# Performance work log

Hardware: AMD Instinct MI355X
Metric: run time of the kernel (lower is better)

## Reference

```python
import jax, jax.numpy as jnp
import numpy as np

N = 50000
E = 800000
DIM_H = 128
EPS = 1e-5


def _glorot(key, shape):
    fan_in, fan_out = shape[0], shape[1]
    lim = np.sqrt(6.0 / (fan_in + fan_out))
    return jax.random.uniform(key, shape, jnp.float32, -lim, lim)


def setup_inputs() -> dict:
    key = jax.random.key(0)
    ks = jax.random.split(key, 12)
    h = jax.random.normal(ks[0], (N, DIM_H), jnp.float32)
    x = jax.random.normal(ks[1], (N, 3), jnp.float32)
    e = jax.random.randint(ks[2], (2, E), 0, N, jnp.int32)
    dx = jax.random.normal(ks[3], (E, 3), jnp.float32)
    d2 = jax.random.uniform(ks[4], (E, 1), jnp.float32)
    # message_layer.phi params: Linear(2*dim_h+1, dim_h), LayerNorm(dim_h), Linear(dim_h, dim_h)
    W1 = _glorot(ks[5], (2 * DIM_H + 1, DIM_H))
    b1 = jnp.zeros((DIM_H,), jnp.float32)
    g1 = jnp.ones((DIM_H,), jnp.float32)
    beta1 = jnp.zeros((DIM_H,), jnp.float32)
    W2 = _glorot(ks[6], (DIM_H, DIM_H))
    b2 = jnp.zeros((DIM_H,), jnp.float32)
    # outer phi params: Linear(dim_h, dim_h), Linear(dim_h, 1)
    W3 = _glorot(ks[7], (DIM_H, DIM_H))
    b3 = jnp.zeros((DIM_H,), jnp.float32)
    W4 = _glorot(ks[8], (DIM_H, 1))
    b4 = jnp.zeros((1,), jnp.float32)
    return {"h": h, "x": x, "e": e, "dx": dx, "d2": d2,
            "W1": W1, "b1": b1, "g1": g1, "beta1": beta1,
            "W2": W2, "b2": b2, "W3": W3, "b3": b3, "W4": W4, "b4": b4}


def _layernorm(z, g, b):
    mu = jnp.mean(z, axis=-1, keepdims=True)
    var = jnp.mean(jnp.square(z - mu), axis=-1, keepdims=True)
    return (z - mu) * jax.lax.rsqrt(var + EPS) * g + b


def reference(h, x, e, dx, d2, W1, b1, g1, beta1, W2, b2, W3, b3, W4, b4):
    ei, ej = e[0], e[1]
    hi = h[ei]                      # [E, dim_h]
    hj = h[ej]                      # [E, dim_h]
    msg = jnp.concatenate((hi, hj, d2), axis=-1)   # [E, 2*dim_h+1]
    msg = jax.nn.silu(msg @ W1 + b1)
    msg = _layernorm(msg, g1, beta1)
    msg = jax.nn.silu(msg @ W2 + b2)               # [E, dim_h]
    scale = jax.nn.silu(msg @ W3 + b3) @ W4 + b4   # [E, 1]
    vec = dx * scale                               # [E, 3]
    agg = jax.ops.segment_sum(vec, ei, num_segments=N)  # [N, 3]
    return x + agg
```

## Files before the change

### kernel.cpp

```cpp
#include <hip/hip_runtime.h>
#include <hip/hip_bf16.h>
#include <cstdint>

#define NN 50000
#define NE 800000
#define DH 128
#define TILES 50000

typedef __bf16 bf16;
typedef __bf16 bf16x8 __attribute__((ext_vector_type(8)));
typedef float  f32x4  __attribute__((ext_vector_type(4)));

__device__ __forceinline__ float fast_silu(float x) {
    float e = __expf(-x);
    return x * __builtin_amdgcn_rcpf(1.0f + e);
}

__global__ void prep_kernel(const float* __restrict__ W1, const float* __restrict__ W2,
                            const float* __restrict__ W3, const float* __restrict__ b1,
                            const float* __restrict__ g1, const float* __restrict__ bt1,
                            const float* __restrict__ b2, const float* __restrict__ b3,
                            const float* __restrict__ W4,
                            bf16* __restrict__ w1aT, bf16* __restrict__ w1bT,
                            bf16* __restrict__ w2T,  bf16* __restrict__ w3T,
                            float* __restrict__ smalls) {
    int i = blockIdx.x * 256 + threadIdx.x;
    int n = i >> 7, k = i & 127;
    w1aT[i] = (bf16)W1[k * DH + n];
    w1bT[i] = (bf16)W1[(k + DH) * DH + n];
    w2T[i]  = (bf16)W2[k * DH + n];
    w3T[i]  = (bf16)W3[k * DH + n];
    if (i < DH) {
        smalls[i]          = W1[256 * DH + i];
        smalls[DH + i]     = b1[i];
        smalls[2 * DH + i] = g1[i];
        smalls[3 * DH + i] = bt1[i];
        smalls[4 * DH + i] = b2[i];
        smalls[5 * DH + i] = b3[i];
        smalls[6 * DH + i] = W4[i];
    }
}

__global__ __launch_bounds__(256) void node_kernel(const float* __restrict__ h,
                                                   const bf16* __restrict__ w1aT,
                                                   const bf16* __restrict__ w1bT,
                                                   bf16* __restrict__ An,
                                                   bf16* __restrict__ Bn) {
    int lane = threadIdx.x & 63, wid = threadIdx.x >> 6;
    int r = lane & 15, g = lane >> 4;
    int wt = blockIdx.x * 4 + wid;
    if (wt >= (NN / 16)) return;
    int base = wt * 16;
    int node = base + r;

    bf16x8 ha[4];
#pragma unroll
    for (int s = 0; s < 4; s++) {
        const float* hp = h + (size_t)node * DH + s * 32 + g * 8;
        float4 p0 = *(const float4*)hp;
        float4 p1 = *(const float4*)(hp + 4);
        ha[s][0] = (bf16)p0.x; ha[s][1] = (bf16)p0.y;
        ha[s][2] = (bf16)p0.z; ha[s][3] = (bf16)p0.w;
        ha[s][4] = (bf16)p1.x; ha[s][5] = (bf16)p1.y;
        ha[s][6] = (bf16)p1.z; ha[s][7] = (bf16)p1.w;
    }
#pragma unroll
    for (int t = 0; t < 16; t++) {
        const bf16* wmat = (t < 8) ? w1aT : w1bT;
        int n = (t & 7) * 16 + r;
        f32x4 acc = {0.f, 0.f, 0.f, 0.f};
#pragma unroll
        for (int s = 0; s < 4; s++) {
            bf16x8 wb = *(const bf16x8*)(wmat + n * DH + s * 32 + g * 8);
            acc = __builtin_amdgcn_mfma_f32_16x16x32_bf16(ha[s], wb, acc, 0, 0, 0);
        }
        bf16* dst = (t < 8) ? An : Bn;
#pragma unroll
        for (int jj = 0; jj < 4; jj++)
            dst[(size_t)(base + g * 4 + jj) * DH + (t & 7) * 16 + r] = (bf16)acc[jj];
    }
}

__global__ void init_kernel(const float* __restrict__ x, float* __restrict__ out, int n) {
    int i = blockIdx.x * 256 + threadIdx.x;
    if (i < n) out[i] = x[i];
}

__global__ __launch_bounds__(512, 2) void edge_kernel(
    const bf16* __restrict__ An, const bf16* __restrict__ Bn,
    const bf16* __restrict__ w2T, const bf16* __restrict__ w3T,
    const float* __restrict__ smalls, const float* __restrict__ b4p,
    const int* __restrict__ e, const float* __restrict__ dxv,
    const float* __restrict__ d2, float* __restrict__ out) {
    __shared__ __align__(16) bf16 sW2[128 * 136];
    __shared__ __align__(16) bf16 sW3[128 * 136];
    __shared__ __align__(16) bf16 sY[8 * 16 * 136];
    __shared__ float sSm[7 * 128];

    int tid = threadIdx.x;
    for (int c = tid; c < 2048; c += 512) {
        int row = c >> 4, col = (c & 15) * 8;
        *(bf16x8*)&sW2[row * 136 + col] = *(const bf16x8*)&w2T[row * 128 + col];
        *(bf16x8*)&sW3[row * 136 + col] = *(const bf16x8*)&w3T[row * 128 + col];
    }
    if (tid < 128) {
#pragma unroll
        for (int a = 0; a < 7; a++) sSm[a * 128 + tid] = smalls[a * 128 + tid];
    }
    __syncthreads();

    const float* s_w1c = sSm;
    const float* s_b1  = sSm + 128;
    const float* s_g1  = sSm + 256;
    const float* s_bt1 = sSm + 384;
    const float* s_b2  = sSm + 512;
    const float* s_b3  = sSm + 640;
    const float* s_W4  = sSm + 768;
    float b4v = b4p[0];

    int lane = tid & 63, wid = tid >> 6;
    int r = lane & 15, g = lane >> 4;
    bf16* yw = &sY[wid * 16 * 136];
    int wgid = blockIdx.x * 8 + wid;
    int nw = gridDim.x * 8;

    for (int tile = wgid; tile < TILES; tile += nw) {
        int base = tile * 16;
        int ei = e[base + r];
        int ej = e[NE + base + r];
        float d2v = d2[base + r];
        const bf16* Ar = An + (size_t)ei * DH;
        const bf16* Br = Bn + (size_t)ej * DH;

        float z[4][8];
#pragma unroll
        for (int s = 0; s < 4; s++) {
            bf16x8 av = *(const bf16x8*)(Ar + s * 32 + g * 8);
            bf16x8 bv = *(const bf16x8*)(Br + s * 32 + g * 8);
#pragma unroll
            for (int j = 0; j < 8; j++) {
                int f = s * 32 + g * 8 + j;
                float zz = (float)av[j] + (float)bv[j] + d2v * s_w1c[f] + s_b1[f];
                z[s][j] = fast_silu(zz);
            }
        }
        float sum = 0.f, sq = 0.f;
#pragma unroll
        for (int s = 0; s < 4; s++)
#pragma unroll
            for (int j = 0; j < 8; j++) { sum += z[s][j]; sq += z[s][j] * z[s][j]; }
        sum += __shfl_xor(sum, 16); sq += __shfl_xor(sq, 16);
        sum += __shfl_xor(sum, 32); sq += __shfl_xor(sq, 32);
        float mu = sum * 0.0078125f;
        float var = sq * 0.0078125f - mu * mu;
        float rs = __builtin_amdgcn_rsqf(var + 1e-5f);

        bf16x8 af[4];
#pragma unroll
        for (int s = 0; s < 4; s++)
#pragma unroll
            for (int j = 0; j < 8; j++) {
                int f = s * 32 + g * 8 + j;
                af[s][j] = (bf16)((z[s][j] - mu) * rs * s_g1[f] + s_bt1[f]);
            }

#pragma unroll
        for (int t = 0; t < 8; t++) {
            f32x4 acc = {0.f, 0.f, 0.f, 0.f};
#pragma unroll
            for (int s = 0; s < 4; s++) {
                bf16x8 wb = *(const bf16x8*)&sW2[(t * 16 + r) * 136 + s * 32 + g * 8];
                acc = __builtin_amdgcn_mfma_f32_16x16x32_bf16(af[s], wb, acc, 0, 0, 0);
            }
            int n = t * 16 + r;
            float b2n = s_b2[n];
#pragma unroll
            for (int jj = 0; jj < 4; jj++)
                yw[(g * 4 + jj) * 136 + n] = (bf16)fast_silu(acc[jj] + b2n);
        }
        bf16x8 a2[4];
#pragma unroll
        for (int s = 0; s < 4; s++)
            a2[s] = *(const bf16x8*)&yw[r * 136 + s * 32 + g * 8];

        float part[4] = {0.f, 0.f, 0.f, 0.f};
#pragma unroll
        for (int t = 0; t < 8; t++) {
            f32x4 acc = {0.f, 0.f, 0.f, 0.f};
#pragma unroll
            for (int s = 0; s < 4; s++) {
                bf16x8 wb = *(const bf16x8*)&sW3[(t * 16 + r) * 136 + s * 32 + g * 8];
                acc = __builtin_amdgcn_mfma_f32_16x16x32_bf16(a2[s], wb, acc, 0, 0, 0);
            }
            int n = t * 16 + r;
            float b3n = s_b3[n], w4n = s_W4[n];
#pragma unroll
            for (int jj = 0; jj < 4; jj++)
                part[jj] += fast_silu(acc[jj] + b3n) * w4n;
        }
#pragma unroll
        for (int jj = 0; jj < 4; jj++) {
            part[jj] += __shfl_xor(part[jj], 1);
            part[jj] += __shfl_xor(part[jj], 2);
            part[jj] += __shfl_xor(part[jj], 4);
            part[jj] += __shfl_xor(part[jj], 8);
        }
#pragma unroll
        for (int jj = 0; jj < 4; jj++) {
            float scale = part[jj] + b4v;
            int m = g * 4 + jj;
            int eim = __shfl(ei, m);
            if (r < 3)
                atomicAdd(&out[(size_t)eim * 3 + r],
                          dxv[(size_t)(base + m) * 3 + r] * scale);
        }
    }
}

extern "C" void kernel_launch(void* const* d_in, const int* in_sizes, int n_in,
                              void* d_out, int out_size, void* d_ws, size_t ws_size,
                              hipStream_t stream) {
    const float* h   = (const float*)d_in[0];
    const float* x   = (const float*)d_in[1];
    const int*   e   = (const int*)d_in[2];
    const float* dxv = (const float*)d_in[3];
    const float* d2  = (const float*)d_in[4];
    const float* W1  = (const float*)d_in[5];
    const float* b1  = (const float*)d_in[6];
    const float* g1  = (const float*)d_in[7];
    const float* bt1 = (const float*)d_in[8];
    const float* W2  = (const float*)d_in[9];
    const float* b2  = (const float*)d_in[10];
    const float* W3  = (const float*)d_in[11];
    const float* b3  = (const float*)d_in[12];
    const float* W4  = (const float*)d_in[13];
    const float* b4  = (const float*)d_in[14];

    char* ws = (char*)d_ws;
    bf16* An    = (bf16*)(ws);
    bf16* Bn    = (bf16*)(ws + 12800000);
    bf16* w1aT  = (bf16*)(ws + 25600000);
    bf16* w1bT  = (bf16*)(ws + 25600000 + 32768);
    bf16* w2T   = (bf16*)(ws + 25600000 + 65536);
    bf16* w3T   = (bf16*)(ws + 25600000 + 98304);
    float* smalls = (float*)(ws + 25600000 + 131072);
    float* out  = (float*)d_out;

    prep_kernel<<<64, 256, 0, stream>>>(W1, W2, W3, b1, g1, bt1, b2, b3, W4,
                                        w1aT, w1bT, w2T, w3T, smalls);
    node_kernel<<<(NN / 16 + 3) / 4, 256, 0, stream>>>(h, w1aT, w1bT, An, Bn);
    init_kernel<<<(NN * 3 + 255) / 256, 256, 0, stream>>>(x, out, NN * 3);
    edge_kernel<<<256, 512, 0, stream>>>(An, Bn, w2T, w3T, smalls, b4,
                                         e, dxv, d2, out);
}
```

Baseline: 411.2 us.

## Drop W3 from LDS, raise edge-kernel occupancy, prefetch indices, compact atomics

Removes the shared-memory copy of W3 and reads it straight from global (L1/L2-cached) memory, cutting LDS use so launch bounds can rise to 4 blocks per CU and the grid can double to 512 blocks. It also software-prefetches the next tile's edge indices and d2 values, and redistributes the scatter-add so all 64 lanes each handle one (edge, coordinate) pair instead of only lanes r<3. The aim is more latency hiding and fewer idle lanes in the atomic phase. The cost is global-memory traffic for W3 in the inner MFMA loop and tighter register limits that could cause spills.

```diff
diff --git a/kernel.cpp b/kernel.cpp
--- a/kernel.cpp
+++ b/kernel.cpp
@@ -86,14 +86,13 @@
     if (i < n) out[i] = x[i];
 }
 
-__global__ __launch_bounds__(512, 2) void edge_kernel(
+__global__ __launch_bounds__(512, 4) void edge_kernel(
     const bf16* __restrict__ An, const bf16* __restrict__ Bn,
     const bf16* __restrict__ w2T, const bf16* __restrict__ w3T,
     const float* __restrict__ smalls, const float* __restrict__ b4p,
     const int* __restrict__ e, const float* __restrict__ dxv,
     const float* __restrict__ d2, float* __restrict__ out) {
     __shared__ __align__(16) bf16 sW2[128 * 136];
-    __shared__ __align__(16) bf16 sW3[128 * 136];
     __shared__ __align__(16) bf16 sY[8 * 16 * 136];
     __shared__ float sSm[7 * 128];
 
@@ -101,7 +100,6 @@
     for (int c = tid; c < 2048; c += 512) {
         int row = c >> 4, col = (c & 15) * 8;
         *(bf16x8*)&sW2[row * 136 + col] = *(const bf16x8*)&w2T[row * 128 + col];
-        *(bf16x8*)&sW3[row * 136 + col] = *(const bf16x8*)&w3T[row * 128 + col];
     }
     if (tid < 128) {
 #pragma unroll
@@ -124,11 +122,26 @@
     int wgid = blockIdx.x * 8 + wid;
     int nw = gridDim.x * 8;
 
-    for (int tile = wgid; tile < TILES; tile += nw) {
+    const bf16* w3base = w3T + r * DH + g * 8;
+
+    int tile = wgid;
+    int ei_c = 0, ej_c = 0; float d2_c = 0.f;
+    if (tile < TILES) {
+        ei_c = e[tile * 16 + r];
+        ej_c = e[NE + tile * 16 + r];
+        d2_c = d2[tile * 16 + r];
+    }
+
+    for (; tile < TILES; tile += nw) {
         int base = tile * 16;
-        int ei = e[base + r];
-        int ej = e[NE + base + r];
-        float d2v = d2[base + r];
+        int ei = ei_c, ej = ej_c;
+        float d2v = d2_c;
+        int nt = tile + nw;
+        if (nt < TILES) {
+            ei_c = e[nt * 16 + r];
+            ej_c = e[NE + nt * 16 + r];
+            d2_c = d2[nt * 16 + r];
+        }
         const bf16* Ar = An + (size_t)ei * DH;
         const bf16* Br = Bn + (size_t)ej * DH;
 
@@ -189,7 +202,7 @@
             f32x4 acc = {0.f, 0.f, 0.f, 0.f};
 #pragma unroll
             for (int s = 0; s < 4; s++) {
-                bf16x8 wb = *(const bf16x8*)&sW3[(t * 16 + r) * 136 + s * 32 + g * 8];
+                bf16x8 wb = *(const bf16x8*)(w3base + t * 16 * DH + s * 32);
                 acc = __builtin_amdgcn_mfma_f32_16x16x32_bf16(a2[s], wb, acc, 0, 0, 0);
             }
             int n = t * 16 + r;
@@ -205,14 +218,16 @@
             part[jj] += __shfl_xor(part[jj], 4);
             part[jj] += __shfl_xor(part[jj], 8);
         }
-#pragma unroll
-        for (int jj = 0; jj < 4; jj++) {
-            float scale = part[jj] + b4v;
-            int m = g * 4 + jj;
+        {
+            int m = lane >> 2, c = lane & 3;
+            int jj = m & 3;
+            float sc = (jj == 0) ? part[0] : (jj == 1) ? part[1]
+                     : (jj == 2) ? part[2] : part[3];
+            float scale = sc + b4v;
             int eim = __shfl(ei, m);
-            if (r < 3)
-                atomicAdd(&out[(size_t)eim * 3 + r],
-                          dxv[(size_t)(base + m) * 3 + r] * scale);
+            if (c < 3)
+                atomicAdd(&out[(size_t)eim * 3 + c],
+                          dxv[(size_t)(base + m) * 3 + c] * scale);
         }
     }
 }
@@ -250,6 +265,6 @@
                                         w1aT, w1bT, w2T, w3T, smalls);
     node_kernel<<<(NN / 16 + 3) / 4, 256, 0, stream>>>(h, w1aT, w1bT, An, Bn);
     init_kernel<<<(NN * 3 + 255) / 256, 256, 0, stream>>>(x, out, NN * 3);
-    edge_kernel<<<256, 512, 0, stream>>>(An, Bn, w2T, w3T, smalls, b4,
+    edge_kernel<<<512, 512, 0, stream>>>(An, Bn, w2T, w3T, smalls, b4,
                                          e, dxv, d2, out);
 }
```

Result: slower. 1.291 ms (+214.0%).

## Bucket-sort edges by source node and prefetch next tile's gathers in edge kernel

Applied to the files above, without the earlier changes.

Adds histogram, scan and scatter kernels that counting-sort edges into buckets of 16 source nodes, so the edge kernel reads An rows and hits atomic targets with better locality. Each wave now processes a contiguous chunk of tiles with a block swizzle and software-prefetches the next tile's indices and An/Bn rows while computing the current one. The atomic epilogue is also reshaped so each lane issues a single atomic. The sort adds several extra launches plus full passes over edge data and extra workspace traffic, and the prefetch raises register pressure.

```diff
diff --git a/kernel.cpp b/kernel.cpp
--- a/kernel.cpp
+++ b/kernel.cpp
@@ -6,6 +6,8 @@
 #define NE 800000
 #define DH 128
 #define TILES 50000
+#define NBUCK 4096
+#define ECHUNK 25
 
 typedef __bf16 bf16;
 typedef __bf16 bf16x8 __attribute__((ext_vector_type(8)));
@@ -41,6 +43,51 @@
     }
 }
 
+__global__ void zero_kernel(int* __restrict__ cnt) {
+    cnt[blockIdx.x * 256 + threadIdx.x] = 0;
+}
+
+__global__ void hist_kernel(const int* __restrict__ e, int* __restrict__ cnt) {
+    int i = blockIdx.x * 256 + threadIdx.x;
+    if (i < NE) atomicAdd(&cnt[e[i] >> 4], 1);
+}
+
+__global__ __launch_bounds__(1024) void scan_kernel(const int* __restrict__ cnt,
+                                                    int* __restrict__ ofs) {
+    __shared__ int buf[1024];
+    int t = threadIdx.x;
+    int c[4], s0 = 0;
+#pragma unroll
+    for (int k = 0; k < 4; k++) { c[k] = cnt[t * 4 + k]; s0 += c[k]; }
+    buf[t] = s0;
+    __syncthreads();
+    for (int off = 1; off < 1024; off <<= 1) {
+        int v = (t >= off) ? buf[t - off] : 0;
+        __syncthreads();
+        buf[t] += v;
+        __syncthreads();
+    }
+    int excl = buf[t] - s0;
+#pragma unroll
+    for (int k = 0; k < 4; k++) { ofs[t * 4 + k] = excl; excl += c[k]; }
+}
+
+__global__ void ssort_kernel(const int* __restrict__ e, const float* __restrict__ d2,
+                             const float* __restrict__ dxv, int* __restrict__ ofs,
+                             int* __restrict__ sei, int* __restrict__ sej,
+                             float* __restrict__ sd2, float* __restrict__ sdx) {
+    int i = blockIdx.x * 256 + threadIdx.x;
+    if (i >= NE) return;
+    int ei = e[i];
+    int pos = atomicAdd(&ofs[ei >> 4], 1);
+    sei[pos] = ei;
+    sej[pos] = e[NE + i];
+    sd2[pos] = d2[i];
+    sdx[pos * 3 + 0] = dxv[i * 3 + 0];
+    sdx[pos * 3 + 1] = dxv[i * 3 + 1];
+    sdx[pos * 3 + 2] = dxv[i * 3 + 2];
+}
+
 __global__ __launch_bounds__(256) void node_kernel(const float* __restrict__ h,
                                                    const bf16* __restrict__ w1aT,
                                                    const bf16* __restrict__ w1bT,
@@ -90,8 +137,9 @@
     const bf16* __restrict__ An, const bf16* __restrict__ Bn,
     const bf16* __restrict__ w2T, const bf16* __restrict__ w3T,
     const float* __restrict__ smalls, const float* __restrict__ b4p,
-    const int* __restrict__ e, const float* __restrict__ dxv,
-    const float* __restrict__ d2, float* __restrict__ out) {
+    const int* __restrict__ sei, const int* __restrict__ sej,
+    const float* __restrict__ sd2, const float* __restrict__ sdx,
+    float* __restrict__ out) {
     __shared__ __align__(16) bf16 sW2[128 * 136];
     __shared__ __align__(16) bf16 sW3[128 * 136];
     __shared__ __align__(16) bf16 sY[8 * 16 * 136];
@@ -121,29 +169,66 @@
     int lane = tid & 63, wid = tid >> 6;
     int r = lane & 15, g = lane >> 4;
     bf16* yw = &sY[wid * 16 * 136];
-    int wgid = blockIdx.x * 8 + wid;
-    int nw = gridDim.x * 8;
-
-    for (int tile = wgid; tile < TILES; tile += nw) {
+
+    int bid = blockIdx.x;
+    int swz = (bid & 7) * 32 + (bid >> 3);
+    int wave_g = swz * 8 + wid;
+    int tile = wave_g * ECHUNK;
+    int tend = tile + ECHUNK;
+    if (tend > TILES) tend = TILES;
+
+    bf16x8 av[4], bv[4];
+    int ei_r = 0, ej_r = 0; float d2_r = 0.f;
+    if (tile < tend) {
+        ei_r = sei[tile * 16 + r];
+        ej_r = sej[tile * 16 + r];
+        d2_r = sd2[tile * 16 + r];
+        const bf16* Ar = An + (size_t)ei_r * DH;
+        const bf16* Br = Bn + (size_t)ej_r * DH;
+#pragma unroll
+        for (int s = 0; s < 4; s++) {
+            av[s] = *(const bf16x8*)(Ar + s * 32 + g * 8);
+            bv[s] = *(const bf16x8*)(Br + s * 32 + g * 8);
+        }
+    }
+
+    for (; tile < tend; ++tile) {
         int base = tile * 16;
-        int ei = e[base + r];
-        int ej = e[NE + base + r];
-        float d2v = d2[base + r];
-        const bf16* Ar = An + (size_t)ei * DH;
-        const bf16* Br = Bn + (size_t)ej * DH;
+        int nt = tile + 1;
+        bool has_n = (nt < tend);
+        int ei_n = 0, ej_n = 0; float d2_n = 0.f;
+        if (has_n) {
+            ei_n = sei[nt * 16 + r];
+            ej_n = sej[nt * 16 + r];
+            d2_n = sd2[nt * 16 + r];
+        }
+        int m = lane >> 2, c3 = lane & 3;
+        float dxm = (c3 < 3) ? sdx[(size_t)(base + m) * 3 + c3] : 0.f;
 
         float z[4][8];
+        float d2v = d2_r;
 #pragma unroll
         for (int s = 0; s < 4; s++) {
-            bf16x8 av = *(const bf16x8*)(Ar + s * 32 + g * 8);
-            bf16x8 bv = *(const bf16x8*)(Br + s * 32 + g * 8);
 #pragma unroll
             for (int j = 0; j < 8; j++) {
                 int f = s * 32 + g * 8 + j;
-                float zz = (float)av[j] + (float)bv[j] + d2v * s_w1c[f] + s_b1[f];
+                float zz = (float)av[s][j] + (float)bv[s][j] + d2v * s_w1c[f] + s_b1[f];
                 z[s][j] = fast_silu(zz);
             }
         }
+        int ei_cur = ei_r;
+
+        if (has_n) {
+            const bf16* Arn = An + (size_t)ei_n * DH;
+            const bf16* Brn = Bn + (size_t)ej_n * DH;
+#pragma unroll
+            for (int s = 0; s < 4; s++) {
+                av[s] = *(const bf16x8*)(Arn + s * 32 + g * 8);
+                bv[s] = *(const bf16x8*)(Brn + s * 32 + g * 8);
+            }
+            ei_r = ei_n; ej_r = ej_n; d2_r = d2_n;
+        }
+
         float sum = 0.f, sq = 0.f;
 #pragma unroll
         for (int s = 0; s < 4; s++)
@@ -205,14 +290,14 @@
             part[jj] += __shfl_xor(part[jj], 4);
             part[jj] += __shfl_xor(part[jj], 8);
         }
-#pragma unroll
-        for (int jj = 0; jj < 4; jj++) {
-            float scale = part[jj] + b4v;
-            int m = g * 4 + jj;
-            int eim = __shfl(ei, m);
-            if (r < 3)
-                atomicAdd(&out[(size_t)eim * 3 + r],
-                          dxv[(size_t)(base + m) * 3 + r] * scale);
+        {
+            int jj = m & 3;
+            float sc = (jj == 0) ? part[0] : (jj == 1) ? part[1]
+                     : (jj == 2) ? part[2] : part[3];
+            float scale = sc + b4v;
+            int eim = __shfl(ei_cur, m);
+            if (c3 < 3)
+                atomicAdd(&out[(size_t)eim * 3 + c3], dxm * scale);
         }
     }
 }
@@ -237,19 +322,30 @@
     const float* b4  = (const float*)d_in[14];
 
     char* ws = (char*)d_ws;
-    bf16* An    = (bf16*)(ws);
-    bf16* Bn    = (bf16*)(ws + 12800000);
-    bf16* w1aT  = (bf16*)(ws + 25600000);
-    bf16* w1bT  = (bf16*)(ws + 25600000 + 32768);
-    bf16* w2T   = (bf16*)(ws + 25600000 + 65536);
-    bf16* w3T   = (bf16*)(ws + 25600000 + 98304);
+    bf16* An     = (bf16*)(ws);
+    bf16* Bn     = (bf16*)(ws + 12800000);
+    bf16* w1aT   = (bf16*)(ws + 25600000);
+    bf16* w1bT   = (bf16*)(ws + 25600000 + 32768);
+    bf16* w2T    = (bf16*)(ws + 25600000 + 65536);
+    bf16* w3T    = (bf16*)(ws + 25600000 + 98304);
     float* smalls = (float*)(ws + 25600000 + 131072);
-    float* out  = (float*)d_out;
-
+    int*   cnt   = (int*)(ws + 25734656);
+    int*   ofs   = (int*)(ws + 25751040);
+    int*   sei   = (int*)(ws + 25767424);
+    int*   sej   = (int*)(ws + 28967424);
+    float* sd2   = (float*)(ws + 32167424);
+    float* sdx   = (float*)(ws + 35367424);
+    float* out   = (float*)d_out;
+
+    zero_kernel<<<16, 256, 0, stream>>>(cnt);
     prep_kernel<<<64, 256, 0, stream>>>(W1, W2, W3, b1, g1, bt1, b2, b3, W4,
                                         w1aT, w1bT, w2T, w3T, smalls);
+    hist_kernel<<<(NE + 255) / 256, 256, 0, stream>>>(e, cnt);
+    scan_kernel<<<1, 1024, 0, stream>>>(cnt, ofs);
+    ssort_kernel<<<(NE + 255) / 256, 256, 0, stream>>>(e, d2, dxv, ofs,
+                                                       sei, sej, sd2, sdx);
     node_kernel<<<(NN / 16 + 3) / 4, 256, 0, stream>>>(h, w1aT, w1bT, An, Bn);
     init_kernel<<<(NN * 3 + 255) / 256, 256, 0, stream>>>(x, out, NN * 3);
     edge_kernel<<<256, 512, 0, stream>>>(An, Bn, w2T, w3T, smalls, b4,
-                                         e, dxv, d2, out);
-}
+                                         sei, sej, sd2, sdx, out);
+}
```

New measurement: 1.094 ms. 166% more time.

## Split edge kernel into gather/layernorm and MLP phases with chunked intermediate buffer

Applied to the files above, without the earlier changes.

The fused edge kernel is split into two kernels. edgeA gathers node projections, applies SiLU and LayerNorm, and writes bf16 activations in MFMA fragment layout to a workspace buffer. edgeB reads those activations and runs the W2/W3 MLP and the scatter atomics. Edges are processed in four chunks so the intermediate stays cache-sized. W3 is now read from global memory instead of LDS, which frees LDS for more occupancy, and the atomic scatter is remapped so 48 lanes issue atomics at once instead of 3 per group across four iterations. The split adds an extra write and read of a 16 MB intermediate plus more launches, in exchange for better latency hiding in each phase.

```diff
diff --git a/kernel.cpp b/kernel.cpp
--- a/kernel.cpp
+++ b/kernel.cpp
@@ -6,6 +6,8 @@
 #define NE 800000
 #define DH 128
 #define TILES 50000
+#define NCHUNK 4
+#define CT (TILES / NCHUNK)
 
 typedef __bf16 bf16;
 typedef __bf16 bf16x8 __attribute__((ext_vector_type(8)));
@@ -86,46 +88,29 @@
     if (i < n) out[i] = x[i];
 }
 
-__global__ __launch_bounds__(512, 2) void edge_kernel(
+__global__ __launch_bounds__(256) void edgeA_kernel(
     const bf16* __restrict__ An, const bf16* __restrict__ Bn,
-    const bf16* __restrict__ w2T, const bf16* __restrict__ w3T,
-    const float* __restrict__ smalls, const float* __restrict__ b4p,
-    const int* __restrict__ e, const float* __restrict__ dxv,
-    const float* __restrict__ d2, float* __restrict__ out) {
-    __shared__ __align__(16) bf16 sW2[128 * 136];
-    __shared__ __align__(16) bf16 sW3[128 * 136];
-    __shared__ __align__(16) bf16 sY[8 * 16 * 136];
-    __shared__ float sSm[7 * 128];
-
+    const float* __restrict__ smalls, const int* __restrict__ e,
+    const float* __restrict__ d2, bf16* __restrict__ Z, int tile0) {
+    __shared__ float sSm[4 * 128];
     int tid = threadIdx.x;
-    for (int c = tid; c < 2048; c += 512) {
-        int row = c >> 4, col = (c & 15) * 8;
-        *(bf16x8*)&sW2[row * 136 + col] = *(const bf16x8*)&w2T[row * 128 + col];
-        *(bf16x8*)&sW3[row * 136 + col] = *(const bf16x8*)&w3T[row * 128 + col];
-    }
     if (tid < 128) {
 #pragma unroll
-        for (int a = 0; a < 7; a++) sSm[a * 128 + tid] = smalls[a * 128 + tid];
+        for (int a = 0; a < 4; a++) sSm[a * 128 + tid] = smalls[a * 128 + tid];
     }
     __syncthreads();
-
     const float* s_w1c = sSm;
     const float* s_b1  = sSm + 128;
     const float* s_g1  = sSm + 256;
     const float* s_bt1 = sSm + 384;
-    const float* s_b2  = sSm + 512;
-    const float* s_b3  = sSm + 640;
-    const float* s_W4  = sSm + 768;
-    float b4v = b4p[0];
 
     int lane = tid & 63, wid = tid >> 6;
     int r = lane & 15, g = lane >> 4;
-    bf16* yw = &sY[wid * 16 * 136];
-    int wgid = blockIdx.x * 8 + wid;
-    int nw = gridDim.x * 8;
-
-    for (int tile = wgid; tile < TILES; tile += nw) {
-        int base = tile * 16;
+    int wgid = blockIdx.x * 4 + wid;
+    int nw = gridDim.x * 4;
+
+    for (int lt = wgid; lt < CT; lt += nw) {
+        int base = (tile0 + lt) * 16;
         int ei = e[base + r];
         int ej = e[NE + base + r];
         float d2v = d2[base + r];
@@ -155,14 +140,60 @@
         float var = sq * 0.0078125f - mu * mu;
         float rs = __builtin_amdgcn_rsqf(var + 1e-5f);
 
-        bf16x8 af[4];
-#pragma unroll
-        for (int s = 0; s < 4; s++)
+        bf16* zp = Z + (size_t)lt * 2048 + g * 128 + r * 8;
+#pragma unroll
+        for (int s = 0; s < 4; s++) {
+            bf16x8 af;
 #pragma unroll
             for (int j = 0; j < 8; j++) {
                 int f = s * 32 + g * 8 + j;
-                af[s][j] = (bf16)((z[s][j] - mu) * rs * s_g1[f] + s_bt1[f]);
-            }
+                af[j] = (bf16)((z[s][j] - mu) * rs * s_g1[f] + s_bt1[f]);
+            }
+            *(bf16x8*)(zp + s * 512) = af;
+        }
+    }
+}
+
+__global__ __launch_bounds__(512, 2) void edgeB_kernel(
+    const bf16* __restrict__ Z, const bf16* __restrict__ w2T,
+    const bf16* __restrict__ w3T, const float* __restrict__ smalls,
+    const float* __restrict__ b4p, const int* __restrict__ e,
+    const float* __restrict__ dxv, float* __restrict__ out, int tile0) {
+    __shared__ __align__(16) bf16 sW2[128 * 136];
+    __shared__ __align__(16) bf16 sY[8 * 16 * 136];
+    __shared__ float sSm[3 * 128];
+
+    int tid = threadIdx.x;
+    for (int c = tid; c < 2048; c += 512) {
+        int row = c >> 4, col = (c & 15) * 8;
+        *(bf16x8*)&sW2[row * 136 + col] = *(const bf16x8*)&w2T[row * 128 + col];
+    }
+    if (tid < 128) {
+#pragma unroll
+        for (int a = 0; a < 3; a++) sSm[a * 128 + tid] = smalls[(4 + a) * 128 + tid];
+    }
+    __syncthreads();
+
+    const float* s_b2 = sSm;
+    const float* s_b3 = sSm + 128;
+    const float* s_W4 = sSm + 256;
+    float b4v = b4p[0];
+
+    int lane = tid & 63, wid = tid >> 6;
+    int r = lane & 15, g = lane >> 4;
+    bf16* yw = &sY[wid * 16 * 136];
+    const bf16* w3base = w3T + r * DH + g * 8;
+    int wgid = blockIdx.x * 8 + wid;
+    int nw = gridDim.x * 8;
+
+    for (int lt = wgid; lt < CT; lt += nw) {
+        int base = (tile0 + lt) * 16;
+        int ei = e[base + r];
+
+        const bf16* zp = Z + (size_t)lt * 2048 + g * 128 + r * 8;
+        bf16x8 af[4];
+#pragma unroll
+        for (int s = 0; s < 4; s++) af[s] = *(const bf16x8*)(zp + s * 512);
 
 #pragma unroll
         for (int t = 0; t < 8; t++) {
@@ -184,12 +215,12 @@
             a2[s] = *(const bf16x8*)&yw[r * 136 + s * 32 + g * 8];
 
         float part[4] = {0.f, 0.f, 0.f, 0.f};
-#pragma unroll
+#pragma unroll 4
         for (int t = 0; t < 8; t++) {
             f32x4 acc = {0.f, 0.f, 0.f, 0.f};
 #pragma unroll
             for (int s = 0; s < 4; s++) {
-                bf16x8 wb = *(const bf16x8*)&sW3[(t * 16 + r) * 136 + s * 32 + g * 8];
+                bf16x8 wb = *(const bf16x8*)(w3base + t * 16 * DH + s * 32);
                 acc = __builtin_amdgcn_mfma_f32_16x16x32_bf16(a2[s], wb, acc, 0, 0, 0);
             }
             int n = t * 16 + r;
@@ -205,14 +236,16 @@
             part[jj] += __shfl_xor(part[jj], 4);
             part[jj] += __shfl_xor(part[jj], 8);
         }
-#pragma unroll
-        for (int jj = 0; jj < 4; jj++) {
-            float scale = part[jj] + b4v;
-            int m = g * 4 + jj;
+        {
+            int m = lane >> 2, c3 = lane & 3;
+            int jj = m & 3;
+            float sc = (jj == 0) ? part[0] : (jj == 1) ? part[1]
+                     : (jj == 2) ? part[2] : part[3];
+            float scale = sc + b4v;
             int eim = __shfl(ei, m);
-            if (r < 3)
-                atomicAdd(&out[(size_t)eim * 3 + r],
-                          dxv[(size_t)(base + m) * 3 + r] * scale);
+            if (c3 < 3)
+                atomicAdd(&out[(size_t)eim * 3 + c3],
+                          dxv[(size_t)(base + m) * 3 + c3] * scale);
         }
     }
 }
@@ -237,19 +270,25 @@
     const float* b4  = (const float*)d_in[14];
 
     char* ws = (char*)d_ws;
-    bf16* An    = (bf16*)(ws);
-    bf16* Bn    = (bf16*)(ws + 12800000);
-    bf16* w1aT  = (bf16*)(ws + 25600000);
-    bf16* w1bT  = (bf16*)(ws + 25600000 + 32768);
-    bf16* w2T   = (bf16*)(ws + 25600000 + 65536);
-    bf16* w3T   = (bf16*)(ws + 25600000 + 98304);
-    float* smalls = (float*)(ws + 25600000 + 131072);
-    float* out  = (float*)d_out;
+    bf16* An     = (bf16*)(ws);
+    bf16* Bn     = (bf16*)(ws + 12800000);
+    bf16* w1aT   = (bf16*)(ws + 25600000);
+    bf16* w1bT   = (bf16*)(ws + 25632768);
+    bf16* w2T    = (bf16*)(ws + 25665536);
+    bf16* w3T    = (bf16*)(ws + 25698304);
+    float* smalls = (float*)(ws + 25731072);
+    bf16* Z      = (bf16*)(ws + 25734656);
+    float* out   = (float*)d_out;
 
     prep_kernel<<<64, 256, 0, stream>>>(W1, W2, W3, b1, g1, bt1, b2, b3, W4,
                                         w1aT, w1bT, w2T, w3T, smalls);
     node_kernel<<<(NN / 16 + 3) / 4, 256, 0, stream>>>(h, w1aT, w1bT, An, Bn);
     init_kernel<<<(NN * 3 + 255) / 256, 256, 0, stream>>>(x, out, NN * 3);
-    edge_kernel<<<256, 512, 0, stream>>>(An, Bn, w2T, w3T, smalls, b4,
-                                         e, dxv, d2, out);
-}
+
+    for (int c = 0; c < NCHUNK; ++c) {
+        int tile0 = c * CT;
+        edgeA_kernel<<<1024, 256, 0, stream>>>(An, Bn, smalls, e, d2, Z, tile0);
+        edgeB_kernel<<<512, 512, 0, stream>>>(Z, w2T, w3T, smalls, b4,
+                                              e, dxv, out, tile0);
+    }
+}
```

Measured after the change: 423.1 us. 2.9% more time.
